# Kernel optimization log

Measured on AMD Instinct MI355X. Metric: run time of the kernel, lower is better.

The kernel has to match this reference:

```python
import jax, jax.numpy as jnp
import numpy as np

SIZE = 768
INNER = 64

def setup_inputs() -> dict:
    key = jax.random.key(0)
    ks = jax.random.split(key, 7)
    emb_input = jax.random.normal(ks[0], (8, 2048, SIZE), dtype=jnp.float32)
    s = 1.0 / np.sqrt(SIZE)
    Wq = jax.random.normal(ks[1], (INNER, SIZE), dtype=jnp.float32) * s
    bq = jax.random.normal(ks[2], (INNER,), dtype=jnp.float32) * 0.01
    Wk = jax.random.normal(ks[3], (INNER, SIZE), dtype=jnp.float32) * s
    bk = jax.random.normal(ks[4], (INNER,), dtype=jnp.float32) * 0.01
    Wv = jax.random.normal(ks[5], (INNER, SIZE), dtype=jnp.float32) * s
    bv = jax.random.normal(ks[6], (INNER,), dtype=jnp.float32) * 0.01
    return {"emb_input": emb_input, "Wq": Wq, "bq": bq, "Wk": Wk, "bk": bk, "Wv": Wv, "bv": bv}

def reference(emb_input, Wq, bq, Wk, bk, Wv, bv):
    # q,k,v: (B,S,inner)
    q = jnp.einsum('bse,ie->bsi', emb_input, Wq) + bq
    k = jnp.einsum('bse,ie->bsi', emb_input, Wk) + bk
    v = jnp.einsum('bse,ie->bsi', emb_input, Wv) + bv
    # NOTE: original scales by sqrt(emb_size), not sqrt(inner_size)
    scale = 1.0 / np.sqrt(SIZE).astype(np.float32)
    attn = jnp.einsum('bqi,bki->bqk', q, k) * scale  # (B,S,S)
    attn = jax.nn.softmax(attn, axis=2)
    # attn @ v, same math as original broadcast-mul-sum but as a matmul
    return jnp.einsum('bqk,bki->bqi', attn, v)
```

## Files before the change

### kernel.cpp

```cpp
#include <hip/hip_runtime.h>
#include <hip/hip_bf16.h>
#include <math.h>

#define B_  8
#define S_  2048
#define E_  768
#define I_  64

typedef __attribute__((ext_vector_type(4))) float f32x4;
typedef __attribute__((ext_vector_type(8))) short short8;
typedef __attribute__((ext_vector_type(4))) short short4v;

static __device__ __forceinline__ short bf16_of(float x) {
    unsigned u = __builtin_bit_cast(unsigned, x);
    u += 0x7fffu + ((u >> 16) & 1u);
    return (short)(u >> 16);
}

static __device__ __forceinline__ unsigned pk2(float lo, float hi) {
    __hip_bfloat162 h = __float22bfloat162_rn(float2{lo, hi});
    unsigned u; __builtin_memcpy(&u, &h, 4);
    return u;
}
static __device__ __forceinline__ short8 pk8(f32x4 a, f32x4 b) {
    union { unsigned u[4]; short8 s; } r;
    r.u[0] = pk2(a[0], a[1]); r.u[1] = pk2(a[2], a[3]);
    r.u[2] = pk2(b[0], b[1]); r.u[3] = pk2(b[2], b[3]);
    return r.s;
}

typedef __attribute__((address_space(1))) const void gv_t;
typedef __attribute__((address_space(3))) void lv_t;
static __device__ __forceinline__ void gload16(const void* g, void* l) {
    __builtin_amdgcn_global_load_lds((gv_t*)g, (lv_t*)l, 16, 0, 0);
}

#define BARRIER()   asm volatile("s_barrier" ::: "memory")
#define VMCNT(n)    asm volatile("s_waitcnt vmcnt(" #n ")" ::: "memory")

__global__ void wconv(const float* __restrict__ Wq, const float* __restrict__ bq,
                      const float* __restrict__ Wk, const float* __restrict__ bk,
                      const float* __restrict__ Wv, const float* __restrict__ bv,
                      short* __restrict__ Wb, float* __restrict__ bb, float qscale) {
    int r = blockIdx.x;
    const float* src; const float* bsrc; float sc;
    if (r < 64)       { src = Wq + r * E_;         bsrc = bq + r;         sc = qscale; }
    else if (r < 128) { src = Wk + (r - 64) * E_;  bsrc = bk + (r - 64);  sc = 1.0f; }
    else              { src = Wv + (r - 128) * E_; bsrc = bv + (r - 128); sc = 1.0f; }
    for (int j = threadIdx.x; j < E_; j += blockDim.x)
        Wb[r * E_ + j] = bf16_of(src[j] * sc);
    if (threadIdx.x == 0) bb[r] = bsrc[0] * sc;
}

__global__ __launch_bounds__(256) void qkv_proj(
    const float* __restrict__ emb, const short* __restrict__ Wb,
    const float* __restrict__ bb,
    short* __restrict__ qb, short* __restrict__ kb, short* __restrict__ vT)
{
    __shared__ float Af[2][32][64];
    __shared__ short Wf[2][192][64];

    const int tid = threadIdx.x, w = tid >> 6, l = tid & 63;
    const int lr = l & 15, rg = l >> 4;
    const int sm = w & 1, sc = w >> 1;
    const int m0 = blockIdx.x * 32;

    f32x4 acc[6];
#pragma unroll
    for (int t = 0; t < 6; ++t) acc[t] = (f32x4){0.f, 0.f, 0.f, 0.f};

    auto STAGE = [&](int ks, int d) {
        char* ab = (char*)&Af[d][0][0] + w * 2048;
#pragma unroll
        for (int i = 0; i < 2; ++i) {
            int r = w * 8 + i * 4 + (l >> 4);
            const float* src = emb + (size_t)(m0 + r) * E_ + ks * 64 + (((l & 15) ^ (r & 15)) << 2);
            gload16(src, ab + i * 1024);
        }
        char* wb2 = (char*)&Wf[d][0][0] + w * 6144;
#pragma unroll
        for (int i = 0; i < 6; ++i) {
            int r = w * 48 + i * 8 + (l >> 3);
            const short* src = Wb + (size_t)r * E_ + ks * 64 + (((l & 7) ^ (r & 7)) << 3);
            gload16(src, wb2 + i * 1024);
        }
    };

    STAGE(0, 0);
    STAGE(1, 1);

    for (int ks = 0; ks < 12; ++ks) {
        const int cur = ks & 1;
        if (ks == 11) { VMCNT(0); } else { VMCNT(8); }
        BARRIER();
#pragma unroll
        for (int h = 0; h < 2; ++h) {
            const int r = sm * 16 + lr;
            const int s0 = (h * 8 + rg * 2) ^ lr;
            const int s1 = (h * 8 + rg * 2 + 1) ^ lr;
            f32x4 a0 = *(const f32x4*)&Af[cur][r][s0 * 4];
            f32x4 a1 = *(const f32x4*)&Af[cur][r][s1 * 4];
            short8 af = pk8(a0, a1);
#pragma unroll
            for (int tt = 0; tt < 6; ++tt) {
                int rw = (sc * 6 + tt) * 16 + lr;
                short8 wf = *(const short8*)&Wf[cur][rw][((h * 4 + rg) ^ (lr & 7)) << 3];
                acc[tt] = __builtin_amdgcn_mfma_f32_16x16x32_bf16(af, wf, acc[tt], 0, 0, 0);
            }
        }
        BARRIER();
        if (ks + 2 < 12) STAGE(ks + 2, cur);
    }

#pragma unroll
    for (int tt = 0; tt < 6; ++tt) {
        int col = sc * 96 + tt * 16 + lr;
        float bias = bb[col];
        int row = m0 + sm * 16 + rg * 4;
        if (col < 64) {
#pragma unroll
            for (int j = 0; j < 4; ++j)
                qb[(size_t)(row + j) * 64 + col] = bf16_of(acc[tt][j] + bias);
        } else if (col < 128) {
#pragma unroll
            for (int j = 0; j < 4; ++j)
                kb[(size_t)(row + j) * 64 + (col - 64)] = bf16_of(acc[tt][j] + bias);
        } else {
            short4v pv;
#pragma unroll
            for (int j = 0; j < 4; ++j) pv[j] = bf16_of(acc[tt][j] + bias);
            int b = row >> 11, s = row & 2047;
            *(short4v*)&vT[((size_t)b * 64 + (col - 128)) * S_ + s] = pv;
        }
    }
}

__global__ __launch_bounds__(512) void flash_attn(
    const short* __restrict__ qb, const short* __restrict__ kb,
    const short* __restrict__ vT, float* __restrict__ out)
{
    __shared__ __align__(16) char smem[81920];
    short (*Kb)[2][64][64] = (short(*)[2][64][64])(smem);
    short (*Vb)[2][64][64] = (short(*)[2][64][64])(smem + 32768);
    short (*plds)[16][64]  = (short(*)[16][64]) (smem + 65536);
    float (*mbuf)[64][16]  = (float(*)[64][16])(smem);
    float (*rsb)[16]       = (float(*)[16])    (smem + 16384);

    const int tid = threadIdx.x, w = tid >> 6, l = tid & 63;
    const int lr = l & 15, rg = l >> 4;
    const int g = w & 3, c = w >> 2;
    const int batch = blockIdx.x & 7;
    const int qt = blockIdx.x >> 3;
    const int qloc0 = qt * 64 + g * 16;

    const short* kbB = kb + (size_t)batch * S_ * 64;
    const short* vTB = vT + (size_t)batch * 64 * S_;

    const int swsrc = ((l & 7) ^ (l >> 3)) << 3;
    auto STAGE = [&](int ks, int d) {
        const int kt = c * 16 + ks;
        const int rl = g * 16 + (l >> 3);
        char* kd = (char*)&Kb[c][d][0][0] + g * 2048;
        gload16(kbB + (size_t)(kt * 64 + rl) * 64 + swsrc, kd);
        gload16(kbB + (size_t)(kt * 64 + rl + 8) * 64 + swsrc, kd + 1024);
        char* vd = (char*)&Vb[c][d][0][0] + g * 2048;
        gload16(vTB + (size_t)rl * S_ + kt * 64 + swsrc, vd);
        gload16(vTB + (size_t)(rl + 8) * S_ + kt * 64 + swsrc, vd + 1024);
    };

    short8 aq0 = *(const short8*)(qb + (size_t)(batch * S_ + qloc0 + lr) * 64 + rg * 8);
    short8 aq1 = *(const short8*)(qb + (size_t)(batch * S_ + qloc0 + lr) * 64 + 32 + rg * 8);

    f32x4 acc[4];
    float rs[4] = {0.f, 0.f, 0.f, 0.f};
#pragma unroll
    for (int n = 0; n < 4; ++n) acc[n] = (f32x4){0.f, 0.f, 0.f, 0.f};

    STAGE(0, 0);
    STAGE(1, 1);

    for (int ks = 0; ks < 16; ++ks) {
        const int cur = ks & 1;
        if (ks == 15) { VMCNT(0); } else { VMCNT(4); }
        BARRIER();

        f32x4 s2[4];
#pragma unroll
        for (int t = 0; t < 4; ++t) {
            const int rk = t * 16 + lr;
            short8 kf0 = *(const short8*)&Kb[c][cur][rk][((0 * 4 + rg) ^ (lr & 7)) << 3];
            short8 kf1 = *(const short8*)&Kb[c][cur][rk][((1 * 4 + rg) ^ (lr & 7)) << 3];
            f32x4 z = (f32x4){0.f, 0.f, 0.f, 0.f};
            z = __builtin_amdgcn_mfma_f32_16x16x32_bf16(aq0, kf0, z, 0, 0, 0);
            s2[t] = __builtin_amdgcn_mfma_f32_16x16x32_bf16(aq1, kf1, z, 0, 0, 0);
        }
        short* pb = &plds[w][0][0];
#pragma unroll
        for (int t = 0; t < 4; ++t) {
            float p0 = __builtin_amdgcn_exp2f(s2[t][0]);
            float p1 = __builtin_amdgcn_exp2f(s2[t][1]);
            float p2 = __builtin_amdgcn_exp2f(s2[t][2]);
            float p3 = __builtin_amdgcn_exp2f(s2[t][3]);
            rs[0] += p0; rs[1] += p1; rs[2] += p2; rs[3] += p3;
            unsigned w0 = pk2(p0, p1), w1 = pk2(p2, p3);
            const int sl = t * 2 + (lr >> 3), bi = lr & 7;
            pb[(rg * 4 + 0) * 64 + ((sl ^ ((rg * 4 + 0) & 7)) << 3) + bi] = (short)w0;
            pb[(rg * 4 + 1) * 64 + ((sl ^ ((rg * 4 + 1) & 7)) << 3) + bi] = (short)(w0 >> 16);
            pb[(rg * 4 + 2) * 64 + ((sl ^ ((rg * 4 + 2) & 7)) << 3) + bi] = (short)w1;
            pb[(rg * 4 + 3) * 64 + ((sl ^ ((rg * 4 + 3) & 7)) << 3) + bi] = (short)(w1 >> 16);
        }
        short8 pa0 = *(const short8*)&pb[lr * 64 + (((0 * 4 + rg) ^ (lr & 7)) << 3)];
        short8 pa1 = *(const short8*)&pb[lr * 64 + (((1 * 4 + rg) ^ (lr & 7)) << 3)];
#pragma unroll
        for (int n = 0; n < 4; ++n) {
            const int ri = n * 16 + lr;
            short8 v0 = *(const short8*)&Vb[c][cur][ri][((0 * 4 + rg) ^ (lr & 7)) << 3];
            short8 v1 = *(const short8*)&Vb[c][cur][ri][((1 * 4 + rg) ^ (lr & 7)) << 3];
            acc[n] = __builtin_amdgcn_mfma_f32_16x16x32_bf16(pa0, v0, acc[n], 0, 0, 0);
            acc[n] = __builtin_amdgcn_mfma_f32_16x16x32_bf16(pa1, v1, acc[n], 0, 0, 0);
        }

        BARRIER();
        if (ks + 2 < 16) STAGE(ks + 2, cur);
    }

#pragma unroll
    for (int m = 1; m < 16; m <<= 1)
#pragma unroll
        for (int j = 0; j < 4; ++j) rs[j] += __shfl_xor(rs[j], m, 64);

    if (c == 1) {
#pragma unroll
        for (int n = 0; n < 4; ++n)
#pragma unroll
            for (int j = 0; j < 4; ++j) mbuf[g][l][n * 4 + j] = acc[n][j];
        if (lr == 0) {
#pragma unroll
            for (int j = 0; j < 4; ++j) rsb[g][rg * 4 + j] = rs[j];
        }
    }
    __syncthreads();
    if (c == 0) {
        const int qrow = batch * S_ + qloc0 + rg * 4;
#pragma unroll
        for (int j = 0; j < 4; ++j) {
            float inv = 1.0f / (rs[j] + rsb[g][rg * 4 + j]);
            float* orow = out + (size_t)(qrow + j) * 64;
#pragma unroll
            for (int n = 0; n < 4; ++n)
                orow[n * 16 + lr] = (acc[n][j] + mbuf[g][l][n * 4 + j]) * inv;
        }
    }
}

extern "C" void kernel_launch(void* const* d_in, const int* in_sizes, int n_in,
                              void* d_out, int out_size, void* d_ws, size_t ws_size,
                              hipStream_t stream) {
    const float* emb = (const float*)d_in[0];
    const float* Wq  = (const float*)d_in[1];
    const float* bq  = (const float*)d_in[2];
    const float* Wk  = (const float*)d_in[3];
    const float* bk  = (const float*)d_in[4];
    const float* Wv  = (const float*)d_in[5];
    const float* bv  = (const float*)d_in[6];
    float* out = (float*)d_out;

    char* ws = (char*)d_ws;
    short* Wb  = (short*)(ws + 0);
    float* bb  = (float*)(ws + 294912);
    short* qb  = (short*)(ws + 295680);
    short* kb  = (short*)(ws + 295680 + 2097152);
    short* vT  = (short*)(ws + 295680 + 2 * 2097152);

    const float qscale = 1.4426950408889634f / sqrtf((float)E_);

    hipLaunchKernelGGL(wconv, dim3(192), dim3(256), 0, stream,
                       Wq, bq, Wk, bk, Wv, bv, Wb, bb, qscale);
    hipLaunchKernelGGL(qkv_proj, dim3(512), dim3(256), 0, stream,
                       emb, Wb, bb, qb, kb, vT);
    hipLaunchKernelGGL(flash_attn, dim3(256), dim3(512), 0, stream,
                       qb, kb, vT, out);
}
```

Baseline: 43.81 us.

## Give each attention wave two 16-row query tiles, halving block threads

The flash attention kernel now uses 256 threads per block (4 waves) instead of 512. Each wave handles 32 query rows as two 16-row MFMA tiles, so every K and V fragment read from LDS is reused twice. Staging loads per thread double and the wait counts are adjusted to match. The aim is to cut LDS traffic per FLOP, at the cost of more registers per wave and fewer waves per block to hide latency.

```diff
diff --git a/kernel.cpp b/kernel.cpp
--- a/kernel.cpp
+++ b/kernel.cpp
@@ -135,23 +135,23 @@
     }
 }
 
-__global__ __launch_bounds__(512) void flash_attn(
+__global__ __launch_bounds__(256) void flash_attn(
     const short* __restrict__ qb, const short* __restrict__ kb,
     const short* __restrict__ vT, float* __restrict__ out)
 {
     __shared__ __align__(16) char smem[81920];
     short (*Kb)[2][64][64] = (short(*)[2][64][64])(smem);
     short (*Vb)[2][64][64] = (short(*)[2][64][64])(smem + 32768);
-    short (*plds)[16][64]  = (short(*)[16][64]) (smem + 65536);
-    float (*mbuf)[64][16]  = (float(*)[64][16])(smem);
-    float (*rsb)[16]       = (float(*)[16])    (smem + 16384);
+    short (*plds)[32][64]  = (short(*)[32][64]) (smem + 65536);
+    float (*mbuf)[64][32]  = (float(*)[64][32])(smem);
+    float (*rsb)[32]       = (float(*)[32])    (smem + 16384);
 
     const int tid = threadIdx.x, w = tid >> 6, l = tid & 63;
     const int lr = l & 15, rg = l >> 4;
-    const int g = w & 3, c = w >> 2;
+    const int g = w & 1, c = w >> 1;
     const int batch = blockIdx.x & 7;
     const int qt = blockIdx.x >> 3;
-    const int qloc0 = qt * 64 + g * 16;
+    const int qloc0 = qt * 64 + g * 32;
 
     const short* kbB = kb + (size_t)batch * S_ * 64;
     const short* vTB = vT + (size_t)batch * 64 * S_;
@@ -159,65 +159,82 @@
     const int swsrc = ((l & 7) ^ (l >> 3)) << 3;
     auto STAGE = [&](int ks, int d) {
         const int kt = c * 16 + ks;
-        const int rl = g * 16 + (l >> 3);
-        char* kd = (char*)&Kb[c][d][0][0] + g * 2048;
-        gload16(kbB + (size_t)(kt * 64 + rl) * 64 + swsrc, kd);
-        gload16(kbB + (size_t)(kt * 64 + rl + 8) * 64 + swsrc, kd + 1024);
-        char* vd = (char*)&Vb[c][d][0][0] + g * 2048;
-        gload16(vTB + (size_t)rl * S_ + kt * 64 + swsrc, vd);
-        gload16(vTB + (size_t)(rl + 8) * S_ + kt * 64 + swsrc, vd + 1024);
+        const int rl = g * 32 + (l >> 3);
+        char* kd = (char*)&Kb[c][d][0][0] + g * 4096;
+        char* vd = (char*)&Vb[c][d][0][0] + g * 4096;
+#pragma unroll
+        for (int i = 0; i < 4; ++i) {
+            gload16(kbB + (size_t)(kt * 64 + rl + i * 8) * 64 + swsrc, kd + i * 1024);
+            gload16(vTB + (size_t)(rl + i * 8) * S_ + kt * 64 + swsrc, vd + i * 1024);
+        }
     };
 
-    short8 aq0 = *(const short8*)(qb + (size_t)(batch * S_ + qloc0 + lr) * 64 + rg * 8);
-    short8 aq1 = *(const short8*)(qb + (size_t)(batch * S_ + qloc0 + lr) * 64 + 32 + rg * 8);
-
-    f32x4 acc[4];
-    float rs[4] = {0.f, 0.f, 0.f, 0.f};
-#pragma unroll
-    for (int n = 0; n < 4; ++n) acc[n] = (f32x4){0.f, 0.f, 0.f, 0.f};
+    short8 aq[2][2];
+#pragma unroll
+    for (int mg = 0; mg < 2; ++mg)
+#pragma unroll
+        for (int h = 0; h < 2; ++h)
+            aq[mg][h] = *(const short8*)(qb + (size_t)(batch * S_ + qloc0 + mg * 16 + lr) * 64 + h * 32 + rg * 8);
+
+    f32x4 acc[2][4];
+    float rs[2][4];
+#pragma unroll
+    for (int mg = 0; mg < 2; ++mg)
+#pragma unroll
+        for (int n = 0; n < 4; ++n) { acc[mg][n] = (f32x4){0.f, 0.f, 0.f, 0.f}; rs[mg][n] = 0.f; }
 
     STAGE(0, 0);
     STAGE(1, 1);
 
     for (int ks = 0; ks < 16; ++ks) {
         const int cur = ks & 1;
-        if (ks == 15) { VMCNT(0); } else { VMCNT(4); }
+        if (ks == 15) { VMCNT(0); } else { VMCNT(8); }
         BARRIER();
 
-        f32x4 s2[4];
+        f32x4 s2[2][4];
 #pragma unroll
         for (int t = 0; t < 4; ++t) {
             const int rk = t * 16 + lr;
             short8 kf0 = *(const short8*)&Kb[c][cur][rk][((0 * 4 + rg) ^ (lr & 7)) << 3];
             short8 kf1 = *(const short8*)&Kb[c][cur][rk][((1 * 4 + rg) ^ (lr & 7)) << 3];
-            f32x4 z = (f32x4){0.f, 0.f, 0.f, 0.f};
-            z = __builtin_amdgcn_mfma_f32_16x16x32_bf16(aq0, kf0, z, 0, 0, 0);
-            s2[t] = __builtin_amdgcn_mfma_f32_16x16x32_bf16(aq1, kf1, z, 0, 0, 0);
-        }
-        short* pb = &plds[w][0][0];
-#pragma unroll
-        for (int t = 0; t < 4; ++t) {
-            float p0 = __builtin_amdgcn_exp2f(s2[t][0]);
-            float p1 = __builtin_amdgcn_exp2f(s2[t][1]);
-            float p2 = __builtin_amdgcn_exp2f(s2[t][2]);
-            float p3 = __builtin_amdgcn_exp2f(s2[t][3]);
-            rs[0] += p0; rs[1] += p1; rs[2] += p2; rs[3] += p3;
-            unsigned w0 = pk2(p0, p1), w1 = pk2(p2, p3);
-            const int sl = t * 2 + (lr >> 3), bi = lr & 7;
-            pb[(rg * 4 + 0) * 64 + ((sl ^ ((rg * 4 + 0) & 7)) << 3) + bi] = (short)w0;
-            pb[(rg * 4 + 1) * 64 + ((sl ^ ((rg * 4 + 1) & 7)) << 3) + bi] = (short)(w0 >> 16);
-            pb[(rg * 4 + 2) * 64 + ((sl ^ ((rg * 4 + 2) & 7)) << 3) + bi] = (short)w1;
-            pb[(rg * 4 + 3) * 64 + ((sl ^ ((rg * 4 + 3) & 7)) << 3) + bi] = (short)(w1 >> 16);
-        }
-        short8 pa0 = *(const short8*)&pb[lr * 64 + (((0 * 4 + rg) ^ (lr & 7)) << 3)];
-        short8 pa1 = *(const short8*)&pb[lr * 64 + (((1 * 4 + rg) ^ (lr & 7)) << 3)];
+#pragma unroll
+            for (int mg = 0; mg < 2; ++mg) {
+                f32x4 z = (f32x4){0.f, 0.f, 0.f, 0.f};
+                z = __builtin_amdgcn_mfma_f32_16x16x32_bf16(aq[mg][0], kf0, z, 0, 0, 0);
+                s2[mg][t] = __builtin_amdgcn_mfma_f32_16x16x32_bf16(aq[mg][1], kf1, z, 0, 0, 0);
+            }
+        }
+        short8 pa[2][2];
+#pragma unroll
+        for (int mg = 0; mg < 2; ++mg) {
+            short* pb = &plds[w][mg * 16][0];
+#pragma unroll
+            for (int t = 0; t < 4; ++t) {
+                float p0 = __builtin_amdgcn_exp2f(s2[mg][t][0]);
+                float p1 = __builtin_amdgcn_exp2f(s2[mg][t][1]);
+                float p2 = __builtin_amdgcn_exp2f(s2[mg][t][2]);
+                float p3 = __builtin_amdgcn_exp2f(s2[mg][t][3]);
+                rs[mg][0] += p0; rs[mg][1] += p1; rs[mg][2] += p2; rs[mg][3] += p3;
+                unsigned w0 = pk2(p0, p1), w1 = pk2(p2, p3);
+                const int sl = t * 2 + (lr >> 3), bi = lr & 7;
+                pb[(rg * 4 + 0) * 64 + ((sl ^ ((rg * 4 + 0) & 7)) << 3) + bi] = (short)w0;
+                pb[(rg * 4 + 1) * 64 + ((sl ^ ((rg * 4 + 1) & 7)) << 3) + bi] = (short)(w0 >> 16);
+                pb[(rg * 4 + 2) * 64 + ((sl ^ ((rg * 4 + 2) & 7)) << 3) + bi] = (short)w1;
+                pb[(rg * 4 + 3) * 64 + ((sl ^ ((rg * 4 + 3) & 7)) << 3) + bi] = (short)(w1 >> 16);
+            }
+            pa[mg][0] = *(const short8*)&pb[lr * 64 + (((0 * 4 + rg) ^ (lr & 7)) << 3)];
+            pa[mg][1] = *(const short8*)&pb[lr * 64 + (((1 * 4 + rg) ^ (lr & 7)) << 3)];
+        }
 #pragma unroll
         for (int n = 0; n < 4; ++n) {
             const int ri = n * 16 + lr;
             short8 v0 = *(const short8*)&Vb[c][cur][ri][((0 * 4 + rg) ^ (lr & 7)) << 3];
             short8 v1 = *(const short8*)&Vb[c][cur][ri][((1 * 4 + rg) ^ (lr & 7)) << 3];
-            acc[n] = __builtin_amdgcn_mfma_f32_16x16x32_bf16(pa0, v0, acc[n], 0, 0, 0);
-            acc[n] = __builtin_amdgcn_mfma_f32_16x16x32_bf16(pa1, v1, acc[n], 0, 0, 0);
+#pragma unroll
+            for (int mg = 0; mg < 2; ++mg) {
+                acc[mg][n] = __builtin_amdgcn_mfma_f32_16x16x32_bf16(pa[mg][0], v0, acc[mg][n], 0, 0, 0);
+                acc[mg][n] = __builtin_amdgcn_mfma_f32_16x16x32_bf16(pa[mg][1], v1, acc[mg][n], 0, 0, 0);
+            }
         }
 
         BARRIER();
@@ -225,30 +242,38 @@
     }
 
 #pragma unroll
-    for (int m = 1; m < 16; m <<= 1)
-#pragma unroll
-        for (int j = 0; j < 4; ++j) rs[j] += __shfl_xor(rs[j], m, 64);
+    for (int mg = 0; mg < 2; ++mg)
+#pragma unroll
+        for (int m = 1; m < 16; m <<= 1)
+#pragma unroll
+            for (int j = 0; j < 4; ++j) rs[mg][j] += __shfl_xor(rs[mg][j], m, 64);
 
     if (c == 1) {
 #pragma unroll
-        for (int n = 0; n < 4; ++n)
-#pragma unroll
-            for (int j = 0; j < 4; ++j) mbuf[g][l][n * 4 + j] = acc[n][j];
-        if (lr == 0) {
-#pragma unroll
-            for (int j = 0; j < 4; ++j) rsb[g][rg * 4 + j] = rs[j];
+        for (int mg = 0; mg < 2; ++mg) {
+#pragma unroll
+            for (int n = 0; n < 4; ++n)
+#pragma unroll
+                for (int j = 0; j < 4; ++j) mbuf[g][l][mg * 16 + n * 4 + j] = acc[mg][n][j];
+            if (lr == 0) {
+#pragma unroll
+                for (int j = 0; j < 4; ++j) rsb[g][mg * 16 + rg * 4 + j] = rs[mg][j];
+            }
         }
     }
     __syncthreads();
     if (c == 0) {
-        const int qrow = batch * S_ + qloc0 + rg * 4;
-#pragma unroll
-        for (int j = 0; j < 4; ++j) {
-            float inv = 1.0f / (rs[j] + rsb[g][rg * 4 + j]);
-            float* orow = out + (size_t)(qrow + j) * 64;
-#pragma unroll
-            for (int n = 0; n < 4; ++n)
-                orow[n * 16 + lr] = (acc[n][j] + mbuf[g][l][n * 4 + j]) * inv;
+#pragma unroll
+        for (int mg = 0; mg < 2; ++mg) {
+            const int qrow = batch * S_ + qloc0 + mg * 16 + rg * 4;
+#pragma unroll
+            for (int j = 0; j < 4; ++j) {
+                float inv = 1.0f / (rs[mg][j] + rsb[g][mg * 16 + rg * 4 + j]);
+                float* orow = out + (size_t)(qrow + j) * 64;
+#pragma unroll
+                for (int n = 0; n < 4; ++n)
+                    orow[n * 16 + lr] = (acc[mg][n][j] + mbuf[g][l][mg * 16 + n * 4 + j]) * inv;
+            }
         }
     }
 }
@@ -278,6 +303,6 @@
                        Wq, bq, Wk, bk, Wv, bv, Wb, bb, qscale);
     hipLaunchKernelGGL(qkv_proj, dim3(512), dim3(256), 0, stream,
                        emb, Wb, bb, qb, kb, vT);
-    hipLaunchKernelGGL(flash_attn, dim3(256), dim3(512), 0, stream,
+    hipLaunchKernelGGL(flash_attn, dim3(256), dim3(256), 0, stream,
                        qb, kb, vT, out);
 }
```

Measured after the change: 47.00 us. +7.3%, slower.
